# Optimization experiments

Hardware: AMD Instinct MI355X
Metric: run time of the kernel (lower is better)

Reference implementation:

```python
import jax, jax.numpy as jnp
import numpy as np

K = 20          # neighbors
EPS = 1e-5      # BatchNorm eps
SLOPE = 0.2     # LeakyReLU negative slope


def setup_inputs() -> dict:
    key = jax.random.key(0)
    ks = jax.random.split(key, 6)
    B, C, N, O = 8, 3, 4096, 64
    x = jax.random.normal(ks[0], (B, C, N), dtype=jnp.float32)
    W = jax.random.normal(ks[1], (O, 2 * C), dtype=jnp.float32) * 0.1  # conv1x1 weight, bias=False
    gamma = 1.0 + 0.1 * jax.random.normal(ks[2], (O,), dtype=jnp.float32)
    beta = 0.1 * jax.random.normal(ks[3], (O,), dtype=jnp.float32)
    mean = 0.1 * jax.random.normal(ks[4], (O,), dtype=jnp.float32)
    var = jax.random.uniform(ks[5], (O,), dtype=jnp.float32, minval=0.5, maxval=1.5)
    return {"x": x, "W": W, "gamma": gamma, "beta": beta, "mean": mean, "var": var}


def reference(x, W, gamma, beta, mean, var):
    # x: [B, C, N]
    B, C, N = x.shape
    xt = jnp.swapaxes(x, 1, 2)                                   # [B, N, C]
    xx = jnp.sum(x * x, axis=1)                                  # [B, N]
    pd = 2.0 * jnp.einsum('bnc,bmc->bnm', xt, xt) - xx[:, :, None] - xx[:, None, :]
    _, idx = jax.lax.top_k(pd, K)                                # [B, N, K] nearest neighbors
    # gather neighbor features per batch
    feat = jax.vmap(lambda f, i: f[i])(xt, idx)                  # [B, N, K, C]
    center = xt[:, :, None, :]                                   # [B, N, 1, C]
    edge = jnp.concatenate(
        [feat - center, jnp.broadcast_to(center, feat.shape)], axis=-1)  # [B, N, K, 2C]
    # 1x1 conv == channel matmul
    y = jnp.einsum('bnkc,oc->bnko', edge, W)                     # [B, N, K, O]
    inv = gamma / jnp.sqrt(var + EPS)                            # fused inference BatchNorm
    y = y * inv + (beta - mean * inv)
    y = jnp.where(y >= 0, y, SLOPE * y)                          # LeakyReLU(0.2)
    y = jnp.max(y, axis=2)                                       # max over k -> [B, N, O]
    return jnp.swapaxes(y, 1, 2)                                 # [B, O, N]
```

## Files before the change

kernel.cpp:

```cpp
#include <hip/hip_runtime.h>
#include <math.h>

#define NPTS 4096
#define KNN  20
#define NOUT 64
#define WPB  4
#define QPW  4
#define QBLK (WPB * QPW)
#define BLKT (WPB * 64)
#define PCAP 128

__device__ __forceinline__ unsigned ord32(float f) {
    unsigned u = __float_as_uint(f);
    int m = ((int)u) >> 31;
    return u ^ ((unsigned)m | 0x80000000u);
}
__device__ __forceinline__ float iord32(unsigned r) {
    unsigned u = (r & 0x80000000u) ? (r ^ 0x80000000u) : ~r;
    return __uint_as_float(u);
}
__device__ __forceinline__ int mbcnt64(unsigned long long m) {
    return __builtin_amdgcn_mbcnt_hi((unsigned)(m >> 32),
           __builtin_amdgcn_mbcnt_lo((unsigned)m, 0));
}

__global__ __launch_bounds__(256) void pack_kernel(const float* __restrict__ x,
                                                   float4* __restrict__ xq) {
    const int i = blockIdx.x * 256 + threadIdx.x;
    const int b = i >> 12, j = i & (NPTS - 1);
    const float* xb = x + (size_t)b * 3 * NPTS;
    const float a0 = xb[j], a1 = xb[NPTS + j], a2 = xb[2 * NPTS + j];
    xq[i] = make_float4(a0, a1, a2, -fmaf(a0, a0, fmaf(a1, a1, a2 * a2)));
}

__global__ __launch_bounds__(BLKT, 6) void edgeconv_kernel(
    const float4* __restrict__ xq,
    const float* __restrict__ Wm,
    const float* __restrict__ gamma,
    const float* __restrict__ beta,
    const float* __restrict__ mean,
    const float* __restrict__ var,
    float* __restrict__ out)
{
    const int bid = blockIdx.x;
    const int b   = bid >> 8;
    const int n0  = (bid & 255) * QBLK;
    const int t    = threadIdx.x;
    const int lane = t & 63;
    const int w    = t >> 6;

    __shared__ unsigned long long pool[QBLK * PCAP];
    __shared__ int cnt[QBLK];

    const float4* xqb = xq + (size_t)b * NPTS;

    if (lane < QPW) cnt[QPW * w + lane] = 0;

    const int na = __builtin_amdgcn_readfirstlane(n0 + QPW * w);
    float q0[QPW], q1[QPW], q2[QPW];
    #pragma unroll
    for (int q = 0; q < QPW; ++q) {
        const float4 pv = xqb[na + q];
        q0[q] = 2.f * pv.x; q1[q] = 2.f * pv.y; q2[q] = 2.f * pv.z;
    }

    float vm0[QPW], vm1[QPW];
    #pragma unroll
    for (int q = 0; q < QPW; ++q) { vm0[q] = -INFINITY; vm1[q] = -INFINITY; }
    #pragma unroll
    for (int g = 0; g < NPTS / 256; ++g) {
        float4 cc[4];
        #pragma unroll
        for (int u = 0; u < 4; ++u) cc[u] = xqb[(g * 4 + u) * 64 + lane];
        #pragma unroll
        for (int u = 0; u < 4; ++u) {
            #pragma unroll
            for (int q = 0; q < QPW; ++q) {
                const float e = fmaf(q0[q], cc[u].x, fmaf(q1[q], cc[u].y, fmaf(q2[q], cc[u].z, cc[u].w)));
                if (g < 8) vm0[q] = fmaxf(vm0[q], e);
                else       vm1[q] = fmaxf(vm1[q], e);
            }
        }
    }

    float Tf[QPW];
    #pragma unroll
    for (int q = 0; q < QPW; ++q) {
        const unsigned h0 = ord32(vm0[q]) >> 16;
        const unsigned h1 = ord32(vm1[q]) >> 16;
        unsigned K = 0;
        #pragma unroll
        for (int bit = 15; bit >= 0; --bit) {
            const unsigned p = K | (1u << bit);
            const int c = __popcll(__ballot(h0 >= p)) + __popcll(__ballot(h1 >= p));
            if (c >= KNN) K = p;
        }
        Tf[q] = iord32(K << 16);
    }

    const int invl = (NPTS - 1) - lane;

    #pragma unroll
    for (int g = 0; g < NPTS / 256; ++g) {
        float4 cc[4];
        #pragma unroll
        for (int u = 0; u < 4; ++u) cc[u] = xqb[(g * 4 + u) * 64 + lane];
        #pragma unroll
        for (int u = 0; u < 4; ++u) {
            const unsigned tag = (unsigned)(invl - (g * 4 + u) * 64);
            #pragma unroll
            for (int q = 0; q < QPW; ++q) {
                const float e = fmaf(q0[q], cc[u].x, fmaf(q1[q], cc[u].y, fmaf(q2[q], cc[u].z, cc[u].w)));
                if (e >= Tf[q]) {
                    const int pos = atomicAdd(&cnt[QPW * w + q], 1);
                    if (pos < PCAP)
                        pool[(QPW * w + q) * PCAP + pos] =
                            ((unsigned long long)ord32(e) << 32) | tag;
                }
            }
        }
    }

    unsigned myidx[QPW];
    #pragma unroll
    for (int q = 0; q < QPW; ++q) {
        const int pr = QPW * w + q;
        unsigned long long* pl = pool + (size_t)pr * PCAP;
        int cw = __builtin_amdgcn_readfirstlane(cnt[pr]);
        if (cw > PCAP) cw = PCAP;

        const unsigned long long e0 = (lane < cw) ? pl[lane] : 0ull;
        const unsigned long long e1 = (lane + 64 < cw) ? pl[lane + 64] : 0ull;
        const unsigned k0 = (unsigned)(e0 >> 32), t0 = (unsigned)e0;
        const unsigned k1 = (unsigned)(e1 >> 32), t1 = (unsigned)e1;

        unsigned K = 0;
        #pragma unroll
        for (int bit = 31; bit >= 0; --bit) {
            const unsigned p = K | (1u << bit);
            const int c = __popcll(__ballot(k0 >= p)) + __popcll(__ballot(k1 >= p));
            if (c >= KNN) K = p;
        }

        unsigned long long g0 = __ballot(k0 > K);
        unsigned long long g1 = __ballot(k1 > K);
        const int m = __popcll(g0) + __popcll(g1);
        unsigned long long s0 = __ballot(k0 == K);
        unsigned long long s1 = __ballot(k1 == K);
        const int r = KNN - m;
        if (__popcll(s0) + __popcll(s1) > r) {
            unsigned TT = 0;
            #pragma unroll
            for (int bit = 11; bit >= 0; --bit) {
                const unsigned p = TT | (1u << bit);
                const int c = __popcll(__ballot(k0 == K && t0 >= p)) +
                              __popcll(__ballot(k1 == K && t1 >= p));
                if (c >= r) TT = p;
            }
            s0 = __ballot(k0 == K && t0 >= TT);
            s1 = __ballot(k1 == K && t1 >= TT);
        }

        unsigned* idxq = (unsigned*)pl;
        if ((g0 >> lane) & 1) idxq[mbcnt64(g0)] = t0;
        if ((g1 >> lane) & 1) idxq[__popcll(g0) + mbcnt64(g1)] = t1;
        if ((s0 >> lane) & 1) idxq[m + mbcnt64(s0)] = t0;
        if ((s1 >> lane) & 1) idxq[m + __popcll(s0) + mbcnt64(s1)] = t1;
        myidx[q] = idxq[(lane < KNN) ? lane : 0];
    }

    __syncthreads();

    const int o = lane;
    const float iv   = gamma[o] / sqrtf(var[o] + 1e-5f);
    const float bias = beta[o] - mean[o] * iv;
    const float* Wr = Wm + o * 6;
    const float w0p = Wr[0] * iv, w1p = Wr[1] * iv, w2p = Wr[2] * iv;
    const float w3p = Wr[3] * iv, w4p = Wr[4] * iv, w5p = Wr[5] * iv;

    float* outT = (float*)pool;
    #pragma unroll
    for (int q = 0; q < QPW; ++q) {
        const float4 pv = xqb[na + q];
        const float basep = fmaf(w3p, pv.x, fmaf(w4p, pv.y, fmaf(w5p, pv.z, bias)));
        const float base2 = basep - fmaf(w0p, pv.x, fmaf(w1p, pv.y, w2p * pv.z));
        float best = -INFINITY;
        #pragma unroll
        for (int k = 0; k < KNN; ++k) {
            const int lk = __builtin_amdgcn_readlane((int)myidx[q], k);
            const int gi = __builtin_amdgcn_readfirstlane((NPTS - 1) - lk);
            const float4 f = xqb[gi];
            float y = fmaf(w0p, f.x, fmaf(w1p, f.y, fmaf(w2p, f.z, base2)));
            y = fmaxf(y, 0.2f * y);
            best = fmaxf(best, y);
        }
        outT[o * (QBLK + 1) + QPW * w + q] = best;
    }
    __syncthreads();

    {
        const int oo = t >> 2, seg = t & 3;
        const int sb = oo * (QBLK + 1) + seg * 4;
        float4 vv;
        vv.x = outT[sb + 0]; vv.y = outT[sb + 1];
        vv.z = outT[sb + 2]; vv.w = outT[sb + 3];
        *(float4*)(out + ((size_t)b * NOUT + oo) * NPTS + n0 + seg * 4) = vv;
    }
}

extern "C" void kernel_launch(void* const* d_in, const int* in_sizes, int n_in,
                              void* d_out, int out_size, void* d_ws, size_t ws_size,
                              hipStream_t stream) {
    const float* x     = (const float*)d_in[0];
    const float* Wm    = (const float*)d_in[1];
    const float* gamma = (const float*)d_in[2];
    const float* beta  = (const float*)d_in[3];
    const float* mean  = (const float*)d_in[4];
    const float* var   = (const float*)d_in[5];
    float* out = (float*)d_out;
    float4* xq = (float4*)d_ws;

    const int B = in_sizes[0] / (3 * NPTS);
    pack_kernel<<<B * NPTS / 256, 256, 0, stream>>>(x, xq);
    const int nblocks = B * (NPTS / QBLK);
    edgeconv_kernel<<<nblocks, BLKT, 0, stream>>>(xq, Wm, gamma, beta, mean, var, out);
}
```

Before: 136.2 us.

## Pack distance FMAs into float2 vectors and give output transpose its own LDS buffer

Rewrites the two distance-scoring passes so that pairs of query points are evaluated with float2 elementwise FMA and max operations, which lets the compiler emit packed FP32 instructions (v_pk_fma_f32) and roughly halve VALU issue in the dominant loops. The output transpose buffer moves out of the candidate pool into a separate shared array, which removes one block-wide barrier. The minimum-waves hint in launch bounds is raised from 6 to 7. The extra LDS array and the higher occupancy target may limit registers or LDS and cause spills, and the candidate-collection branch still works per scalar lane.

Measured after the change: 154.1 us. 1.13x slower.

```diff
diff --git a/kernel.cpp b/kernel.cpp
--- a/kernel.cpp
+++ b/kernel.cpp
@@ -10,6 +10,8 @@
 #define BLKT (WPB * 64)
 #define PCAP 128
 
+typedef float v2f __attribute__((ext_vector_type(2)));
+
 __device__ __forceinline__ unsigned ord32(float f) {
     unsigned u = __float_as_uint(f);
     int m = ((int)u) >> 31;
@@ -33,7 +35,7 @@
     xq[i] = make_float4(a0, a1, a2, -fmaf(a0, a0, fmaf(a1, a1, a2 * a2)));
 }
 
-__global__ __launch_bounds__(BLKT, 6) void edgeconv_kernel(
+__global__ __launch_bounds__(BLKT, 7) void edgeconv_kernel(
     const float4* __restrict__ xq,
     const float* __restrict__ Wm,
     const float* __restrict__ gamma,
@@ -50,6 +52,7 @@
     const int w    = t >> 6;
 
     __shared__ unsigned long long pool[QBLK * PCAP];
+    __shared__ float outT[NOUT * (QBLK + 1)];
     __shared__ int cnt[QBLK];
 
     const float4* xqb = xq + (size_t)b * NPTS;
@@ -57,16 +60,19 @@
     if (lane < QPW) cnt[QPW * w + lane] = 0;
 
     const int na = __builtin_amdgcn_readfirstlane(n0 + QPW * w);
-    float q0[QPW], q1[QPW], q2[QPW];
-    #pragma unroll
-    for (int q = 0; q < QPW; ++q) {
-        const float4 pv = xqb[na + q];
-        q0[q] = 2.f * pv.x; q1[q] = 2.f * pv.y; q2[q] = 2.f * pv.z;
-    }
-
-    float vm0[QPW], vm1[QPW];
-    #pragma unroll
-    for (int q = 0; q < QPW; ++q) { vm0[q] = -INFINITY; vm1[q] = -INFINITY; }
+    const float4 pvA = xqb[na + 0];
+    const float4 pvB = xqb[na + 1];
+    const float4 pvC = xqb[na + 2];
+    const float4 pvD = xqb[na + 3];
+    const v2f q0p = {2.f * pvA.x, 2.f * pvB.x};
+    const v2f q1p = {2.f * pvA.y, 2.f * pvB.y};
+    const v2f q2p = {2.f * pvA.z, 2.f * pvB.z};
+    const v2f q0q = {2.f * pvC.x, 2.f * pvD.x};
+    const v2f q1q = {2.f * pvC.y, 2.f * pvD.y};
+    const v2f q2q = {2.f * pvC.z, 2.f * pvD.z};
+
+    v2f vm0p = {-INFINITY, -INFINITY}, vm1p = vm0p;
+    v2f vm0q = vm0p, vm1q = vm0p;
     #pragma unroll
     for (int g = 0; g < NPTS / 256; ++g) {
         float4 cc[4];
@@ -74,20 +80,28 @@
         for (int u = 0; u < 4; ++u) cc[u] = xqb[(g * 4 + u) * 64 + lane];
         #pragma unroll
         for (int u = 0; u < 4; ++u) {
-            #pragma unroll
-            for (int q = 0; q < QPW; ++q) {
-                const float e = fmaf(q0[q], cc[u].x, fmaf(q1[q], cc[u].y, fmaf(q2[q], cc[u].z, cc[u].w)));
-                if (g < 8) vm0[q] = fmaxf(vm0[q], e);
-                else       vm1[q] = fmaxf(vm1[q], e);
-            }
+            const v2f cx = {cc[u].x, cc[u].x}, cy = {cc[u].y, cc[u].y};
+            const v2f cz = {cc[u].z, cc[u].z}, cw = {cc[u].w, cc[u].w};
+            const v2f ep = __builtin_elementwise_fma(q0p, cx,
+                           __builtin_elementwise_fma(q1p, cy,
+                           __builtin_elementwise_fma(q2p, cz, cw)));
+            const v2f eq = __builtin_elementwise_fma(q0q, cx,
+                           __builtin_elementwise_fma(q1q, cy,
+                           __builtin_elementwise_fma(q2q, cz, cw)));
+            if (g < 8) { vm0p = __builtin_elementwise_max(vm0p, ep);
+                         vm0q = __builtin_elementwise_max(vm0q, eq); }
+            else       { vm1p = __builtin_elementwise_max(vm1p, ep);
+                         vm1q = __builtin_elementwise_max(vm1q, eq); }
         }
     }
 
     float Tf[QPW];
+    const float vm0s[QPW] = {vm0p.x, vm0p.y, vm0q.x, vm0q.y};
+    const float vm1s[QPW] = {vm1p.x, vm1p.y, vm1q.x, vm1q.y};
     #pragma unroll
     for (int q = 0; q < QPW; ++q) {
-        const unsigned h0 = ord32(vm0[q]) >> 16;
-        const unsigned h1 = ord32(vm1[q]) >> 16;
+        const unsigned h0 = ord32(vm0s[q]) >> 16;
+        const unsigned h1 = ord32(vm1s[q]) >> 16;
         unsigned K = 0;
         #pragma unroll
         for (int bit = 15; bit >= 0; --bit) {
@@ -97,6 +111,8 @@
         }
         Tf[q] = iord32(K << 16);
     }
+    const v2f Tp = {Tf[0], Tf[1]};
+    const v2f Tq = {Tf[2], Tf[3]};
 
     const int invl = (NPTS - 1) - lane;
 
@@ -107,15 +123,24 @@
         for (int u = 0; u < 4; ++u) cc[u] = xqb[(g * 4 + u) * 64 + lane];
         #pragma unroll
         for (int u = 0; u < 4; ++u) {
+            const v2f cx = {cc[u].x, cc[u].x}, cy = {cc[u].y, cc[u].y};
+            const v2f cz = {cc[u].z, cc[u].z}, cw = {cc[u].w, cc[u].w};
+            const v2f ep = __builtin_elementwise_fma(q0p, cx,
+                           __builtin_elementwise_fma(q1p, cy,
+                           __builtin_elementwise_fma(q2p, cz, cw)));
+            const v2f eq = __builtin_elementwise_fma(q0q, cx,
+                           __builtin_elementwise_fma(q1q, cy,
+                           __builtin_elementwise_fma(q2q, cz, cw)));
             const unsigned tag = (unsigned)(invl - (g * 4 + u) * 64);
+            const float es[QPW] = {ep.x, ep.y, eq.x, eq.y};
+            const float ts[QPW] = {Tp.x, Tp.y, Tq.x, Tq.y};
             #pragma unroll
             for (int q = 0; q < QPW; ++q) {
-                const float e = fmaf(q0[q], cc[u].x, fmaf(q1[q], cc[u].y, fmaf(q2[q], cc[u].z, cc[u].w)));
-                if (e >= Tf[q]) {
+                if (es[q] >= ts[q]) {
                     const int pos = atomicAdd(&cnt[QPW * w + q], 1);
                     if (pos < PCAP)
                         pool[(QPW * w + q) * PCAP + pos] =
-                            ((unsigned long long)ord32(e) << 32) | tag;
+                            ((unsigned long long)ord32(es[q]) << 32) | tag;
                 }
             }
         }
@@ -169,8 +194,6 @@
         myidx[q] = idxq[(lane < KNN) ? lane : 0];
     }
 
-    __syncthreads();
-
     const int o = lane;
     const float iv   = gamma[o] / sqrtf(var[o] + 1e-5f);
     const float bias = beta[o] - mean[o] * iv;
@@ -178,7 +201,6 @@
     const float w0p = Wr[0] * iv, w1p = Wr[1] * iv, w2p = Wr[2] * iv;
     const float w3p = Wr[3] * iv, w4p = Wr[4] * iv, w5p = Wr[5] * iv;
 
-    float* outT = (float*)pool;
     #pragma unroll
     for (int q = 0; q < QPW; ++q) {
         const float4 pv = xqb[na + q];
@@ -196,6 +218,7 @@
         }
         outT[o * (QBLK + 1) + QPW * w + q] = best;
     }
+
     __syncthreads();
 
     {
```
